# Kernel optimization log

Hardware: AMD Instinct MI355X
Metric: run time of the kernel (lower is better)

## Reference

```python
import jax, jax.numpy as jnp
import numpy as np

BETA_2 = 1.0
LAMBDA_2 = 1.0


def _segment_logsumexp(x, seg, num_segments):
    # numerically stable segment logsumexp; empty segments -> 0.0
    m = jax.ops.segment_max(x, seg, num_segments=num_segments)
    m_safe = jnp.where(jnp.isfinite(m), m, 0.0)
    s = jax.ops.segment_sum(jnp.exp(x - m_safe[seg]), seg, num_segments=num_segments)
    lse = m_safe + jnp.log(s)
    return jnp.where(s > 0, lse, 0.0)


def setup_inputs() -> dict:
    key = jax.random.key(0)
    k1, k2, k3, k4, k5 = jax.random.split(key, 5)
    num_nodes, d, num_edges, num_graphs = 100000, 64, 3200000, 256
    Q2 = jax.random.normal(k1, (num_nodes, d), dtype=jnp.float32)
    K2 = jax.random.normal(k2, (num_nodes, d), dtype=jnp.float32)
    c_2 = jax.random.randint(k3, (num_edges,), 0, num_nodes)
    u_2 = jax.random.randint(k4, (num_edges,), 0, num_nodes)
    batch = jnp.sort(jax.random.randint(k5, (num_nodes,), 0, num_graphs))
    return {"Q2": Q2, "K2": K2, "c_2": c_2, "u_2": u_2, "batch": batch,
            "num_graphs": num_graphs}


def reference(Q2, K2, c_2, u_2, batch, num_graphs):
    num_nodes, d = Q2.shape
    scale = d ** 0.5
    # pairwise dot over edges: [E]
    ell_2 = jnp.sum(Q2[c_2] * K2[u_2], axis=-1) / scale
    # segment logsumexp grouped by destination node c: [N]
    lse_2 = _segment_logsumexp(BETA_2 * ell_2, c_2, num_nodes)
    # scatter-add per-node lse into per-graph energy: [G]
    graph_lse = jax.ops.segment_sum(lse_2, batch, num_segments=num_graphs)
    E = (LAMBDA_2 / BETA_2) * graph_lse
    return E
```

## Files before the change

### kernel.cpp

```cpp
#include <hip/hip_runtime.h>
#include <hip/hip_fp8.h>
#include <math.h>

typedef __attribute__((ext_vector_type(2))) float fv2;

#if defined(__has_builtin)
#  if __has_builtin(__builtin_amdgcn_cvt_pk_f32_fp8) && \
      __has_builtin(__builtin_amdgcn_cvt_pk_fp8_f32)
#    define PE_HAVE_FP8_BUILTINS 1
#  endif
#endif

#define MAX_NBP 512
#define NPB 256
#define NPB_SHIFT 8
#define B2_EPT 16
#define B2_CHUNK (B2_EPT * 256)
#define CPB 4

__device__ __forceinline__ unsigned pack4_fp8(float a, float b, float c, float d) {
#ifdef PE_HAVE_FP8_BUILTINS
    int w = 0;
    w = __builtin_amdgcn_cvt_pk_fp8_f32(a, b, w, false);
    w = __builtin_amdgcn_cvt_pk_fp8_f32(c, d, w, true);
    return (unsigned)w;
#else
    unsigned r = 0;
    r |= (unsigned)__hip_fp8_e4m3(a).__x;
    r |= (unsigned)__hip_fp8_e4m3(b).__x << 8;
    r |= (unsigned)__hip_fp8_e4m3(c).__x << 16;
    r |= (unsigned)__hip_fp8_e4m3(d).__x << 24;
    return r;
#endif
}

__device__ __forceinline__ float dot4w_fp8(unsigned qa, unsigned ka, float acc) {
#ifdef PE_HAVE_FP8_BUILTINS
    fv2 q0 = __builtin_amdgcn_cvt_pk_f32_fp8((int)qa, false);
    fv2 q1 = __builtin_amdgcn_cvt_pk_f32_fp8((int)qa, true);
    fv2 k0 = __builtin_amdgcn_cvt_pk_f32_fp8((int)ka, false);
    fv2 k1 = __builtin_amdgcn_cvt_pk_f32_fp8((int)ka, true);
    acc = fmaf(q0.x, k0.x, acc);
    acc = fmaf(q0.y, k0.y, acc);
    acc = fmaf(q1.x, k1.x, acc);
    acc = fmaf(q1.y, k1.y, acc);
    return acc;
#else
#pragma unroll
    for (int j = 0; j < 4; ++j) {
        __hip_fp8_e4m3 qv, kv;
        qv.__x = (qa >> (8 * j)) & 0xff;
        kv.__x = (ka >> (8 * j)) & 0xff;
        acc = fmaf((float)qv, (float)kv, acc);
    }
    return acc;
#endif
}

__device__ __forceinline__ float dot16_fp8(const uint4& q, const uint4& k) {
    float d = 0.0f;
    d = dot4w_fp8(q.x, k.x, d);
    d = dot4w_fp8(q.y, k.y, d);
    d = dot4w_fp8(q.z, k.z, d);
    d = dot4w_fp8(q.w, k.w, d);
    return d;
}

__device__ __forceinline__ float red4(float d) {
    d += __shfl_xor(d, 1, 64);
    d += __shfl_xor(d, 2, 64);
    return d;
}

__global__ __launch_bounds__(256) void pe_convcount_kernel(
    const float* __restrict__ Q,
    const float* __restrict__ K,
    unsigned* __restrict__ Qq,
    unsigned* __restrict__ Kq,
    float* __restrict__ node_sum,
    float* __restrict__ out,
    const int* __restrict__ c,
    unsigned* __restrict__ cnt,
    int n4, int num_nodes, int num_graphs, int num_edges,
    int nbp, int nblk, int nconv) {
    __shared__ unsigned h[MAX_NBP];
    const int tid = threadIdx.x;

    if (blockIdx.x < nconv) {
        const int i = blockIdx.x * 256 + tid;
        if (i < num_nodes) node_sum[i] = 0.0f;
        if (i < num_graphs) out[i] = 0.0f;
        if (i >= n4) return;
        const float4 q = ((const float4*)Q)[i];
        const float4 k = ((const float4*)K)[i];
        Qq[i] = pack4_fp8(q.x, q.y, q.z, q.w);
        Kq[i] = pack4_fp8(k.x, k.y, k.z, k.w);
        return;
    }

    const int blk = blockIdx.x - nconv;
    for (int b = tid; b < MAX_NBP; b += 256) h[b] = 0u;
    __syncthreads();

    const int estart = blk * B2_CHUNK;
    const int ecount = min(B2_CHUNK, num_edges - estart);
    const int n4e = ecount >> 2;
    const int4* c4 = (const int4*)(c + estart);
    for (int k = tid; k < n4e; k += 256) {
        const int4 v = c4[k];
        atomicAdd(&h[v.x >> NPB_SHIFT], 1u);
        atomicAdd(&h[v.y >> NPB_SHIFT], 1u);
        atomicAdd(&h[v.z >> NPB_SHIFT], 1u);
        atomicAdd(&h[v.w >> NPB_SHIFT], 1u);
    }
    for (int e = (n4e << 2) + tid; e < ecount; e += 256)
        atomicAdd(&h[c[estart + e] >> NPB_SHIFT], 1u);
    __syncthreads();

    for (int b = tid; b < nbp; b += 256)
        cnt[(size_t)blk * nbp + b] = h[b];
}

__global__ __launch_bounds__(256) void pe_matscan_kernel(
    unsigned* __restrict__ cnt,
    unsigned* __restrict__ bin_cnt,
    int nblk, int nbp) {
    __shared__ unsigned wsum[4][16];
    const int t = threadIdx.x;
    const int lane = t & 63;
    const int w = t >> 6;
    const int col0 = blockIdx.x * 16;

    unsigned carry[16];
#pragma unroll
    for (int i = 0; i < 16; ++i) carry[i] = 0u;

    for (int t0 = 0; t0 < nblk; t0 += 256) {
        const int blk = t0 + t;
        unsigned v[16], orig[16];
        if (blk < nblk) {
            const uint4* p = (const uint4*)(cnt + (size_t)blk * nbp + col0);
            const uint4 a = p[0], b = p[1], cc = p[2], dd = p[3];
            v[0]=a.x;  v[1]=a.y;  v[2]=a.z;  v[3]=a.w;
            v[4]=b.x;  v[5]=b.y;  v[6]=b.z;  v[7]=b.w;
            v[8]=cc.x; v[9]=cc.y; v[10]=cc.z; v[11]=cc.w;
            v[12]=dd.x; v[13]=dd.y; v[14]=dd.z; v[15]=dd.w;
        } else {
#pragma unroll
            for (int i = 0; i < 16; ++i) v[i] = 0u;
        }
#pragma unroll
        for (int i = 0; i < 16; ++i) orig[i] = v[i];

#pragma unroll
        for (int off = 1; off < 64; off <<= 1) {
            unsigned nv[16];
#pragma unroll
            for (int i = 0; i < 16; ++i) nv[i] = __shfl_up(v[i], off, 64);
            if (lane >= off) {
#pragma unroll
                for (int i = 0; i < 16; ++i) v[i] += nv[i];
            }
        }
        if (lane == 63) {
#pragma unroll
            for (int i = 0; i < 16; ++i) wsum[w][i] = v[i];
        }
        __syncthreads();

        unsigned woff[16];
#pragma unroll
        for (int i = 0; i < 16; ++i) woff[i] = 0u;
        for (int ww = 0; ww < w; ++ww)
#pragma unroll
            for (int i = 0; i < 16; ++i) woff[i] += wsum[ww][i];

        if (blk < nblk) {
            uint4 o[4];
            unsigned e[16];
#pragma unroll
            for (int i = 0; i < 16; ++i) e[i] = carry[i] + woff[i] + v[i] - orig[i];
            o[0] = make_uint4(e[0], e[1], e[2], e[3]);
            o[1] = make_uint4(e[4], e[5], e[6], e[7]);
            o[2] = make_uint4(e[8], e[9], e[10], e[11]);
            o[3] = make_uint4(e[12], e[13], e[14], e[15]);
            uint4* p = (uint4*)(cnt + (size_t)blk * nbp + col0);
            p[0] = o[0]; p[1] = o[1]; p[2] = o[2]; p[3] = o[3];
        }

#pragma unroll
        for (int i = 0; i < 16; ++i)
            carry[i] += wsum[0][i] + wsum[1][i] + wsum[2][i] + wsum[3][i];
        __syncthreads();
    }

    if (t == 0) {
#pragma unroll
        for (int i = 0; i < 16; ++i) bin_cnt[col0 + i] = carry[i];
    }
}

__global__ __launch_bounds__(1024) void pe_scan_kernel(
    const unsigned* __restrict__ bin_cnt,
    unsigned* __restrict__ bin_base,
    int nb) {
    __shared__ unsigned s[1024];
    const int t = threadIdx.x;
    const unsigned v = (t < nb) ? bin_cnt[t] : 0u;
    s[t] = v;
    __syncthreads();
    for (int off = 1; off < 1024; off <<= 1) {
        const unsigned mine = s[t];
        const unsigned add = (t >= off) ? s[t - off] : 0u;
        __syncthreads();
        s[t] = mine + add;
        __syncthreads();
    }
    if (t < nb) bin_base[t] = s[t] - v;
    if (t == 0) bin_base[nb] = s[1023];
}

__global__ __launch_bounds__(256) void pe_binify_kernel(
    const int* __restrict__ c,
    const int* __restrict__ u,
    const unsigned* __restrict__ cnt,
    const unsigned* __restrict__ bin_base,
    unsigned* __restrict__ recs,
    int num_edges, int nb, int nbp, int nblk) {
    __shared__ unsigned rank[MAX_NBP];
    __shared__ unsigned lstart[MAX_NBP];
    __shared__ unsigned basesh[MAX_NBP];
    __shared__ unsigned srec[B2_CHUNK];
    __shared__ unsigned short sbuk[B2_CHUNK];
    __shared__ unsigned wtot[4];

    const int tid = threadIdx.x;
    const int blk = blockIdx.x;
    const int estart = blk * B2_CHUNK;
    const int ecount = min(B2_CHUNK, num_edges - estart);

    for (int b = tid; b < MAX_NBP; b += 256) rank[b] = 0u;
    for (int b = tid; b < nb; b += 256)
        basesh[b] = bin_base[b] + cnt[(size_t)blk * nbp + b];
    __syncthreads();

    unsigned rw[B2_EPT];
    int rb[B2_EPT];
    unsigned rr[B2_EPT];

    if (ecount == B2_CHUNK) {
        const int4* c4 = (const int4*)(c + estart);
        const int4* u4 = (const int4*)(u + estart);
#pragma unroll
        for (int jj = 0; jj < 4; ++jj) {
            const int k = jj * 256 + tid;
            const int4 cv = c4[k];
            const int4 uv = u4[k];
            const int j = jj * 4;
            rb[j + 0] = cv.x >> NPB_SHIFT;
            rb[j + 1] = cv.y >> NPB_SHIFT;
            rb[j + 2] = cv.z >> NPB_SHIFT;
            rb[j + 3] = cv.w >> NPB_SHIFT;
            rw[j + 0] = ((unsigned)uv.x << NPB_SHIFT) | (unsigned)(cv.x & (NPB - 1));
            rw[j + 1] = ((unsigned)uv.y << NPB_SHIFT) | (unsigned)(cv.y & (NPB - 1));
            rw[j + 2] = ((unsigned)uv.z << NPB_SHIFT) | (unsigned)(cv.z & (NPB - 1));
            rw[j + 3] = ((unsigned)uv.w << NPB_SHIFT) | (unsigned)(cv.w & (NPB - 1));
            rr[j + 0] = atomicAdd(&rank[rb[j + 0]], 1u);
            rr[j + 1] = atomicAdd(&rank[rb[j + 1]], 1u);
            rr[j + 2] = atomicAdd(&rank[rb[j + 2]], 1u);
            rr[j + 3] = atomicAdd(&rank[rb[j + 3]], 1u);
        }
    } else {
#pragma unroll
        for (int j = 0; j < B2_EPT; ++j) {
            rb[j] = -1;
            const int e = estart + j * 256 + tid;
            if (e < num_edges) {
                const int cc = c[e];
                const int uu = u[e];
                rb[j] = cc >> NPB_SHIFT;
                rw[j] = ((unsigned)uu << NPB_SHIFT) | (unsigned)(cc & (NPB - 1));
                rr[j] = atomicAdd(&rank[rb[j]], 1u);
            }
        }
    }
    __syncthreads();

    {
        const int b2 = tid * 2;
        const unsigned v0 = rank[b2 + 0];
        const unsigned v1 = rank[b2 + 1];
        const unsigned tsum = v0 + v1;
        unsigned incl = tsum;
        const int lane = tid & 63;
#pragma unroll
        for (int off = 1; off < 64; off <<= 1) {
            const unsigned nv = __shfl_up(incl, off, 64);
            if (lane >= off) incl += nv;
        }
        if (lane == 63) wtot[tid >> 6] = incl;
        __syncthreads();
        unsigned woff = 0;
        const int w = tid >> 6;
        for (int i = 0; i < w; ++i) woff += wtot[i];
        const unsigned run = woff + incl - tsum;
        lstart[b2 + 0] = run;
        lstart[b2 + 1] = run + v0;
    }
    __syncthreads();

#pragma unroll
    for (int j = 0; j < B2_EPT; ++j) {
        if (rb[j] >= 0) {
            const unsigned pos = lstart[rb[j]] + rr[j];
            srec[pos] = rw[j];
            sbuk[pos] = (unsigned short)rb[j];
        }
    }
    __syncthreads();

    for (int i = tid; i < ecount; i += 256) {
        const int b = sbuk[i];
        recs[basesh[b] + (unsigned)i - lstart[b]] = srec[i];
    }
}

__global__ __launch_bounds__(256) void pe_dotred_kernel(
    const unsigned* __restrict__ Qq,
    const unsigned* __restrict__ Kq,
    const unsigned* __restrict__ recs,
    const unsigned* __restrict__ bin_base,
    float* __restrict__ node_sum,
    int num_nodes, int nb) {
    __shared__ uint4 qlds[NPB * 4];
    __shared__ float acc[NPB];

    const int g = blockIdx.x;
    const int B = g >> 2;
    const int chunk = g & 3;
    if (B >= nb) return;

    const int t = threadIdx.x;
    const int gteam = t >> 2;
    const int sub = t & 3;
    const float inv_scale = 0.125f;

    const int nrows = min(NPB, num_nodes - B * NPB);
    const uint4* qsrc = (const uint4*)Qq + (size_t)B * NPB * 4;
    for (int i = t; i < nrows * 4; i += 256) qlds[i] = qsrc[i];
    acc[t] = 0.0f;
    __syncthreads();

    const unsigned s0 = bin_base[B];
    const unsigned len = bin_base[B + 1] - s0;
    const unsigned r0 = s0 + (unsigned)(((unsigned long long)len * chunk) / CPB);
    const unsigned r1 = s0 + (unsigned)(((unsigned long long)len * (chunk + 1)) / CPB);

    unsigned i = r0 + gteam;
    for (; i + 64 < r1; i += 128) {
        const unsigned recA = recs[i];
        const unsigned recB = recs[i + 64];
        const unsigned uA = recA >> NPB_SHIFT, lA = recA & (NPB - 1);
        const unsigned uB = recB >> NPB_SHIFT, lB = recB & (NPB - 1);
        const uint4 kA = *(const uint4*)(Kq + (size_t)uA * 16 + sub * 4);
        const uint4 kB = *(const uint4*)(Kq + (size_t)uB * 16 + sub * 4);
        const uint4 qA = qlds[lA * 4 + sub];
        const uint4 qB = qlds[lB * 4 + sub];
        const float dA = red4(dot16_fp8(qA, kA));
        const float dB = red4(dot16_fp8(qB, kB));
        if (sub == 0) {
            atomicAdd(&acc[lA], __expf(dA * inv_scale));
            atomicAdd(&acc[lB], __expf(dB * inv_scale));
        }
    }
    for (; i < r1; i += 64) {
        const unsigned rec = recs[i];
        const unsigned uu = rec >> NPB_SHIFT, ll = rec & (NPB - 1);
        const uint4 k = *(const uint4*)(Kq + (size_t)uu * 16 + sub * 4);
        const uint4 q4 = qlds[ll * 4 + sub];
        const float d = red4(dot16_fp8(q4, k));
        if (sub == 0) atomicAdd(&acc[ll], __expf(d * inv_scale));
    }
    __syncthreads();

    if (t < nrows && acc[t] != 0.0f)
        atomicAdd(&node_sum[B * NPB + t], acc[t]);
}

__global__ __launch_bounds__(256) void pe_node_kernel(
    const float* __restrict__ node_sum,
    const int* __restrict__ batch,
    float* __restrict__ out,
    int num_nodes) {
    const int n = blockIdx.x * blockDim.x + threadIdx.x;
    const bool valid = (n < num_nodes);
    const int nc = valid ? n : (num_nodes - 1);

    const float s = valid ? node_sum[nc] : 0.0f;
    float lse = (s > 0.0f) ? logf(s) : 0.0f;
    if (!valid) lse = 0.0f;
    const int b = batch[nc];

    const int b0 = __shfl(b, 0, 64);
    const bool uniform = __all(b == b0);
    if (uniform) {
        lse += __shfl_xor(lse, 1, 64);
        lse += __shfl_xor(lse, 2, 64);
        lse += __shfl_xor(lse, 4, 64);
        lse += __shfl_xor(lse, 8, 64);
        lse += __shfl_xor(lse, 16, 64);
        lse += __shfl_xor(lse, 32, 64);
        if ((threadIdx.x & 63) == 0 && lse != 0.0f) {
            atomicAdd(&out[b0], lse);
        }
    } else {
        if (valid && lse != 0.0f) {
            atomicAdd(&out[b], lse);
        }
    }
}


__global__ __launch_bounds__(256) void pe_convert_kernel(
    const float* __restrict__ Q,
    const float* __restrict__ K,
    unsigned* __restrict__ Qq,
    unsigned* __restrict__ Kq,
    float* __restrict__ node_sum,
    float* __restrict__ out,
    int n4, int num_nodes, int num_graphs) {
    const int i = blockIdx.x * blockDim.x + threadIdx.x;
    if (i < num_nodes) node_sum[i] = 0.0f;
    if (i < num_graphs) out[i] = 0.0f;
    if (i >= n4) return;
    const float4 q = ((const float4*)Q)[i];
    const float4 k = ((const float4*)K)[i];
    Qq[i] = pack4_fp8(q.x, q.y, q.z, q.w);
    Kq[i] = pack4_fp8(k.x, k.y, k.z, k.w);
}

__global__ __launch_bounds__(256) void pe_edge_kernel(
    const unsigned* __restrict__ Qq,
    const unsigned* __restrict__ Kq,
    const int* __restrict__ c,
    const int* __restrict__ u,
    float* __restrict__ node_sum,
    int num_edges) {
    const int tid = blockIdx.x * blockDim.x + threadIdx.x;
    const int group = tid >> 2;
    const int sub = tid & 3;
    const int ngroups = (gridDim.x * blockDim.x) >> 2;
    const float inv_scale = 0.125f;

    const int E4 = num_edges & ~3;

    for (int base = group * 4; base < E4; base += ngroups * 4) {
        const int4 ci = *(const int4*)(c + base);
        const int4 ui = *(const int4*)(u + base);

        const uint4 q0 = *(const uint4*)(Qq + (size_t)ci.x * 16 + sub * 4);
        const uint4 q1 = *(const uint4*)(Qq + (size_t)ci.y * 16 + sub * 4);
        const uint4 q2 = *(const uint4*)(Qq + (size_t)ci.z * 16 + sub * 4);
        const uint4 q3 = *(const uint4*)(Qq + (size_t)ci.w * 16 + sub * 4);
        const uint4 k0 = *(const uint4*)(Kq + (size_t)ui.x * 16 + sub * 4);
        const uint4 k1 = *(const uint4*)(Kq + (size_t)ui.y * 16 + sub * 4);
        const uint4 k2 = *(const uint4*)(Kq + (size_t)ui.z * 16 + sub * 4);
        const uint4 k3 = *(const uint4*)(Kq + (size_t)ui.w * 16 + sub * 4);

        float d0 = red4(dot16_fp8(q0, k0));
        float d1 = red4(dot16_fp8(q1, k1));
        float d2 = red4(dot16_fp8(q2, k2));
        float d3 = red4(dot16_fp8(q3, k3));

        const float dsel = (sub == 0) ? d0 : (sub == 1) ? d1 : (sub == 2) ? d2 : d3;
        const int csel = (sub == 0) ? ci.x : (sub == 1) ? ci.y : (sub == 2) ? ci.z : ci.w;
        atomicAdd(&node_sum[csel], __expf(dsel * inv_scale));
    }

    for (int e = E4 + group; e < num_edges; e += ngroups) {
        const int cc = c[e];
        const int uu = u[e];
        const uint4 q = *(const uint4*)(Qq + (size_t)cc * 16 + sub * 4);
        const uint4 k = *(const uint4*)(Kq + (size_t)uu * 16 + sub * 4);
        float d = red4(dot16_fp8(q, k));
        if (sub == 0) atomicAdd(&node_sum[cc], __expf(d * inv_scale));
    }
}

extern "C" void kernel_launch(void* const* d_in, const int* in_sizes, int n_in,
                              void* d_out, int out_size, void* d_ws, size_t ws_size,
                              hipStream_t stream) {
    const float* Q2 = (const float*)d_in[0];
    const float* K2 = (const float*)d_in[1];
    const int* c_2 = (const int*)d_in[2];
    const int* u_2 = (const int*)d_in[3];
    const int* batch = (const int*)d_in[4];

    const int num_nodes = in_sizes[4];
    const int num_edges = in_sizes[2];
    const int num_graphs = out_size;
    const int d = in_sizes[0] / num_nodes;
    const size_t row_elems = (size_t)num_nodes * d;
    const size_t row_bytes = row_elems;

    const int nb = (num_nodes + NPB - 1) >> NPB_SHIFT;
    const int nbp = (nb + 15) & ~15;
    const int nblk = (num_edges + B2_CHUNK - 1) / B2_CHUNK;

    unsigned* Qq = (unsigned*)d_ws;
    unsigned* Kq = Qq + row_bytes / 4;
    unsigned* meta = Kq + row_bytes / 4;
    unsigned* bin_cnt = meta;
    unsigned* bin_base = meta + MAX_NBP;
    float* node_sum_b = (float*)(meta + 2 * MAX_NBP + 16);
    const size_t ns_pad = ((size_t)num_nodes + 15) & ~(size_t)15;
    unsigned* recs = (unsigned*)node_sum_b + ns_pad;
    unsigned* cnt = recs + num_edges;
    float* node_sum_f = (float*)meta;
    float* out = (float*)d_out;

    const size_t need_binned = row_bytes * 2 + (size_t)(2 * MAX_NBP + 16) * 4 +
                               ns_pad * 4 + (size_t)num_edges * 4 +
                               (size_t)nblk * nbp * 4;
    const bool use_binned = (nb <= MAX_NBP) && (ws_size >= need_binned) &&
                            (d == 64) && (num_nodes <= (1 << 23));

    float* node_sum = use_binned ? node_sum_b : node_sum_f;
    const int n4 = (int)(row_elems / 4);
    const int nconv = (n4 + 255) / 256;

    if (use_binned) {
        pe_convcount_kernel<<<nconv + nblk, 256, 0, stream>>>(
            Q2, K2, Qq, Kq, node_sum, out, c_2, cnt,
            n4, num_nodes, num_graphs, num_edges, nbp, nblk, nconv);
        pe_matscan_kernel<<<nbp / 16, 256, 0, stream>>>(cnt, bin_cnt,
                                                        nblk, nbp);
        pe_scan_kernel<<<1, 1024, 0, stream>>>(bin_cnt, bin_base, nb);
        pe_binify_kernel<<<nblk, 256, 0, stream>>>(c_2, u_2, cnt,
                                                   bin_base, recs,
                                                   num_edges, nb, nbp, nblk);
        pe_dotred_kernel<<<nb * CPB, 256, 0, stream>>>(Qq, Kq, recs,
                                                       bin_base,
                                                       node_sum, num_nodes, nb);
    } else {
        pe_convert_kernel<<<nconv, 256, 0, stream>>>(
            Q2, K2, Qq, Kq, node_sum, out, n4, num_nodes, num_graphs);
        pe_edge_kernel<<<8192, 256, 0, stream>>>(Qq, Kq, c_2, u_2,
                                                 node_sum, num_edges);
    }

    {
        const int block = 256;
        const int grid = (num_nodes + block - 1) / block;
        pe_node_kernel<<<grid, block, 0, stream>>>(node_sum, batch, out,
                                                   num_nodes);
    }
}
```

Before: 204.0 us.

## Fold bucket scan into consumers and fuse node LSE into dotred via last-block flag

Drops the standalone single-block scan kernel: binify and dotred each recompute the exclusive prefix over bucket counts in shared memory. Fuses the per-node log and per-graph reduction into the dot-reduce kernel, where the last of the CPB chunk blocks for a bucket (found with an atomic counter) finishes that bucket's nodes. It also reorders the convcount grid so the counting blocks come first. This removes two kernel launches and their serialization gaps, at the cost of redundant scan work in every block and an extra fence plus atomic per block.

```diff
diff --git a/kernel.cpp b/kernel.cpp
--- a/kernel.cpp
+++ b/kernel.cpp
@@ -79,17 +79,19 @@
     unsigned* __restrict__ Kq,
     float* __restrict__ node_sum,
     float* __restrict__ out,
+    unsigned* __restrict__ bucket_done,
     const int* __restrict__ c,
     unsigned* __restrict__ cnt,
     int n4, int num_nodes, int num_graphs, int num_edges,
-    int nbp, int nblk, int nconv) {
+    int nbp, int nblk) {
     __shared__ unsigned h[MAX_NBP];
     const int tid = threadIdx.x;
 
-    if (blockIdx.x < nconv) {
-        const int i = blockIdx.x * 256 + tid;
+    if (blockIdx.x >= nblk) {
+        const int i = (blockIdx.x - nblk) * 256 + tid;
         if (i < num_nodes) node_sum[i] = 0.0f;
         if (i < num_graphs) out[i] = 0.0f;
+        if (i < MAX_NBP) bucket_done[i] = 0u;
         if (i >= n4) return;
         const float4 q = ((const float4*)Q)[i];
         const float4 k = ((const float4*)K)[i];
@@ -98,7 +100,7 @@
         return;
     }
 
-    const int blk = blockIdx.x - nconv;
+    const int blk = blockIdx.x;
     for (int b = tid; b < MAX_NBP; b += 256) h[b] = 0u;
     __syncthreads();
 
@@ -200,31 +202,11 @@
     }
 }
 
-__global__ __launch_bounds__(1024) void pe_scan_kernel(
-    const unsigned* __restrict__ bin_cnt,
-    unsigned* __restrict__ bin_base,
-    int nb) {
-    __shared__ unsigned s[1024];
-    const int t = threadIdx.x;
-    const unsigned v = (t < nb) ? bin_cnt[t] : 0u;
-    s[t] = v;
-    __syncthreads();
-    for (int off = 1; off < 1024; off <<= 1) {
-        const unsigned mine = s[t];
-        const unsigned add = (t >= off) ? s[t - off] : 0u;
-        __syncthreads();
-        s[t] = mine + add;
-        __syncthreads();
-    }
-    if (t < nb) bin_base[t] = s[t] - v;
-    if (t == 0) bin_base[nb] = s[1023];
-}
-
 __global__ __launch_bounds__(256) void pe_binify_kernel(
     const int* __restrict__ c,
     const int* __restrict__ u,
     const unsigned* __restrict__ cnt,
-    const unsigned* __restrict__ bin_base,
+    const unsigned* __restrict__ bin_cnt,
     unsigned* __restrict__ recs,
     int num_edges, int nb, int nbp, int nblk) {
     __shared__ unsigned rank[MAX_NBP];
@@ -232,6 +214,7 @@
     __shared__ unsigned basesh[MAX_NBP];
     __shared__ unsigned srec[B2_CHUNK];
     __shared__ unsigned short sbuk[B2_CHUNK];
+    __shared__ unsigned sc[256];
     __shared__ unsigned wtot[4];
 
     const int tid = threadIdx.x;
@@ -240,8 +223,26 @@
     const int ecount = min(B2_CHUNK, num_edges - estart);
 
     for (int b = tid; b < MAX_NBP; b += 256) rank[b] = 0u;
-    for (int b = tid; b < nb; b += 256)
-        basesh[b] = bin_base[b] + cnt[(size_t)blk * nbp + b];
+
+    {
+        const int i0 = 2 * tid, i1 = 2 * tid + 1;
+        const unsigned v0 = (i0 < nb) ? bin_cnt[i0] : 0u;
+        const unsigned v1 = (i1 < nb) ? bin_cnt[i1] : 0u;
+        const unsigned p = v0 + v1;
+        sc[tid] = p;
+        __syncthreads();
+        for (int off = 1; off < 256; off <<= 1) {
+            const unsigned mine = sc[tid];
+            const unsigned add = (tid >= off) ? sc[tid - off] : 0u;
+            __syncthreads();
+            sc[tid] = mine + add;
+            __syncthreads();
+        }
+        const unsigned excl = sc[tid] - p;
+        const unsigned* cntrow = cnt + (size_t)blk * nbp;
+        if (i0 < nb) basesh[i0] = excl + cntrow[i0];
+        if (i1 < nb) basesh[i1] = excl + v0 + cntrow[i1];
+    }
     __syncthreads();
 
     unsigned rw[B2_EPT];
@@ -329,16 +330,21 @@
     const unsigned* __restrict__ Qq,
     const unsigned* __restrict__ Kq,
     const unsigned* __restrict__ recs,
-    const unsigned* __restrict__ bin_base,
+    const unsigned* __restrict__ bin_cnt,
     float* __restrict__ node_sum,
+    const int* __restrict__ batch,
+    float* __restrict__ out,
+    unsigned* __restrict__ bucket_done,
     int num_nodes, int nb) {
     __shared__ uint4 qlds[NPB * 4];
     __shared__ float acc[NPB];
+    __shared__ unsigned sc[256];
+    __shared__ unsigned sbase[MAX_NBP + 1];
+    __shared__ unsigned lastflag;
 
     const int g = blockIdx.x;
     const int B = g >> 2;
     const int chunk = g & 3;
-    if (B >= nb) return;
 
     const int t = threadIdx.x;
     const int gteam = t >> 2;
@@ -349,10 +355,30 @@
     const uint4* qsrc = (const uint4*)Qq + (size_t)B * NPB * 4;
     for (int i = t; i < nrows * 4; i += 256) qlds[i] = qsrc[i];
     acc[t] = 0.0f;
-    __syncthreads();
-
-    const unsigned s0 = bin_base[B];
-    const unsigned len = bin_base[B + 1] - s0;
+
+    {
+        const int i0 = 2 * t, i1 = 2 * t + 1;
+        const unsigned v0 = (i0 < nb) ? bin_cnt[i0] : 0u;
+        const unsigned v1 = (i1 < nb) ? bin_cnt[i1] : 0u;
+        const unsigned p = v0 + v1;
+        sc[t] = p;
+        __syncthreads();
+        for (int off = 1; off < 256; off <<= 1) {
+            const unsigned mine = sc[t];
+            const unsigned add = (t >= off) ? sc[t - off] : 0u;
+            __syncthreads();
+            sc[t] = mine + add;
+            __syncthreads();
+        }
+        const unsigned excl = sc[t] - p;
+        sbase[i0] = excl;
+        sbase[i1] = excl + v0;
+        if (t == 255) sbase[512] = sc[255];
+    }
+    __syncthreads();
+
+    const unsigned s0 = sbase[B];
+    const unsigned len = sbase[B + 1] - s0;
     const unsigned r0 = s0 + (unsigned)(((unsigned long long)len * chunk) / CPB);
     const unsigned r1 = s0 + (unsigned)(((unsigned long long)len * (chunk + 1)) / CPB);
 
@@ -385,6 +411,36 @@
 
     if (t < nrows && acc[t] != 0.0f)
         atomicAdd(&node_sum[B * NPB + t], acc[t]);
+    __threadfence();
+    __syncthreads();
+
+    if (t == 0)
+        lastflag = (atomicAdd(&bucket_done[B], 1u) == CPB - 1) ? 1u : 0u;
+    __syncthreads();
+
+    if (lastflag) {
+        const int node = B * NPB + t;
+        const bool valid = t < nrows;
+        float s = 0.0f;
+        if (valid) s = atomicAdd(&node_sum[node], 0.0f);
+        float lse = (valid && s > 0.0f) ? logf(s) : 0.0f;
+        const int nc = valid ? node : (num_nodes - 1);
+        const int b = batch[nc];
+
+        const int b0 = __shfl(b, 0, 64);
+        const bool uniform = __all(b == b0);
+        if (uniform) {
+            lse += __shfl_xor(lse, 1, 64);
+            lse += __shfl_xor(lse, 2, 64);
+            lse += __shfl_xor(lse, 4, 64);
+            lse += __shfl_xor(lse, 8, 64);
+            lse += __shfl_xor(lse, 16, 64);
+            lse += __shfl_xor(lse, 32, 64);
+            if ((t & 63) == 0 && lse != 0.0f) atomicAdd(&out[b0], lse);
+        } else {
+            if (valid && lse != 0.0f) atomicAdd(&out[b], lse);
+        }
+    }
 }
 
 __global__ __launch_bounds__(256) void pe_node_kernel(
@@ -511,7 +567,7 @@
     unsigned* Kq = Qq + row_bytes / 4;
     unsigned* meta = Kq + row_bytes / 4;
     unsigned* bin_cnt = meta;
-    unsigned* bin_base = meta + MAX_NBP;
+    unsigned* bucket_done = meta + MAX_NBP;
     float* node_sum_b = (float*)(meta + 2 * MAX_NBP + 16);
     const size_t ns_pad = ((size_t)num_nodes + 15) & ~(size_t)15;
     unsigned* recs = (unsigned*)node_sum_b + ns_pad;
@@ -530,29 +586,24 @@
     const int nconv = (n4 + 255) / 256;
 
     if (use_binned) {
-        pe_convcount_kernel<<<nconv + nblk, 256, 0, stream>>>(
-            Q2, K2, Qq, Kq, node_sum, out, c_2, cnt,
-            n4, num_nodes, num_graphs, num_edges, nbp, nblk, nconv);
+        pe_convcount_kernel<<<nblk + nconv, 256, 0, stream>>>(
+            Q2, K2, Qq, Kq, node_sum, out, bucket_done, c_2, cnt,
+            n4, num_nodes, num_graphs, num_edges, nbp, nblk);
         pe_matscan_kernel<<<nbp / 16, 256, 0, stream>>>(cnt, bin_cnt,
                                                         nblk, nbp);
-        pe_scan_kernel<<<1, 1024, 0, stream>>>(bin_cnt, bin_base, nb);
         pe_binify_kernel<<<nblk, 256, 0, stream>>>(c_2, u_2, cnt,
-                                                   bin_base, recs,
+                                                   bin_cnt, recs,
                                                    num_edges, nb, nbp, nblk);
-        pe_dotred_kernel<<<nb * CPB, 256, 0, stream>>>(Qq, Kq, recs,
-                                                       bin_base,
-                                                       node_sum, num_nodes, nb);
+        pe_dotred_kernel<<<nb * CPB, 256, 0, stream>>>(
+            Qq, Kq, recs, bin_cnt, node_sum, batch, out, bucket_done,
+            num_nodes, nb);
     } else {
         pe_convert_kernel<<<nconv, 256, 0, stream>>>(
             Q2, K2, Qq, Kq, node_sum, out, n4, num_nodes, num_graphs);
         pe_edge_kernel<<<8192, 256, 0, stream>>>(Qq, Kq, c_2, u_2,
                                                  node_sum, num_edges);
-    }
-
-    {
-        const int block = 256;
-        const int grid = (num_nodes + block - 1) / block;
-        pe_node_kernel<<<grid, block, 0, stream>>>(node_sum, batch, out,
-                                                   num_nodes);
-    }
-}
+        const int grid = (num_nodes + 255) / 256;
+        pe_node_kernel<<<grid, 256, 0, stream>>>(node_sum, batch, out,
+                                                 num_nodes);
+    }
+}
```

Result: slower. 331.5 us (+62.5%).
